# Optimization experiments

Hardware: AMD Instinct MI355X
Metric: run time of the kernel (lower is better)

The kernel has to match this reference:

```python
import jax, jax.numpy as jnp
import numpy as np

H = 16
EPS = 1e-5

def _layernorm(x, gamma, beta):
    mu = jnp.mean(x, axis=-1, keepdims=True)
    var = jnp.var(x, axis=-1, keepdims=True)
    return (x - mu) * jax.lax.rsqrt(var + EPS) * gamma + beta

def setup_inputs() -> dict:
    key = jax.random.key(0)
    ks = jax.random.split(key, 5)
    B, T, E = 4, 2048, 1024
    D = E // H
    return {
        "x": jax.random.normal(ks[0], (B, T, E), dtype=jnp.float32),
        "Wqkv": jax.random.normal(ks[1], (E, 3 * E), dtype=jnp.float32) * (E ** -0.5),
        "bqkv": jax.random.normal(ks[2], (3 * E,), dtype=jnp.float32) * 0.02,
        "q_gamma": jnp.ones((D,), jnp.float32),
        "q_beta": jnp.zeros((D,), jnp.float32),
        "k_gamma": jnp.ones((D,), jnp.float32),
        "k_beta": jnp.zeros((D,), jnp.float32),
        "Wproj": jax.random.normal(ks[3], (E, E), dtype=jnp.float32) * (E ** -0.5),
        "bproj": jnp.zeros((E,), jnp.float32),
    }

def reference(x, Wqkv, bqkv, q_gamma, q_beta, k_gamma, k_beta, Wproj, bproj):
    B, T, E = x.shape
    D = E // H
    qkv = x @ Wqkv + bqkv                      # [B,T,3E]
    q, k, v = jnp.split(qkv, 3, axis=-1)
    # b t (h d) -> b h t d
    to_heads = lambda a: a.reshape(B, T, H, D).transpose(0, 2, 1, 3)
    q, k, v = to_heads(q), to_heads(k), to_heads(v)
    q = _layernorm(q, q_gamma, q_beta)
    k = _layernorm(k, k_gamma, k_beta)
    scale = 1.0 / jnp.sqrt(jnp.float32(D))
    scores = jnp.einsum('bhtd,bhsd->bhts', q, k) * scale   # [B,H,T,T]
    attn = jax.nn.softmax(scores, axis=-1)
    y = jnp.einsum('bhts,bhsd->bhtd', attn, v)             # [B,H,T,D]
    y = y.transpose(0, 2, 1, 3).reshape(B, T, E)           # b h t d -> b t (h d)
    return y @ Wproj + bproj
```

## Files before the change

kernel.cpp:

```cpp
#include <hip/hip_runtime.h>

#define Hn  16
#define Dh  64
#define Bb  4
#define Tn  2048
#define En  1024
#define Mn  8192
#define N1  3072
#define Kn  1024

typedef __attribute__((ext_vector_type(8)))  short  short8;
typedef __attribute__((ext_vector_type(4)))  short  short4v;
typedef __attribute__((ext_vector_type(4)))  float  f32x4;
typedef __attribute__((ext_vector_type(8)))  __bf16 bf16x8;

__device__ __forceinline__ float b2f(short s) {
  unsigned u = ((unsigned)(unsigned short)s) << 16;
  return __builtin_bit_cast(float, u);
}
__device__ __forceinline__ short f2b(float f) {
  unsigned u = __builtin_bit_cast(unsigned, f);
  u += 0x7fffu + ((u >> 16) & 1u);
  return (short)(u >> 16);
}
__device__ __forceinline__ f32x4 mfma16(short8 a, short8 b, f32x4 c) {
  return __builtin_amdgcn_mfma_f32_16x16x32_bf16(
      __builtin_bit_cast(bf16x8, a), __builtin_bit_cast(bf16x8, b), c, 0, 0, 0);
}
__device__ __forceinline__ void gload16(const void* g, void* l) {
  __builtin_amdgcn_global_load_lds(
      (const __attribute__((address_space(1))) unsigned int*)g,
      (__attribute__((address_space(3))) unsigned int*)l, 16, 0, 0);
}

__global__ __launch_bounds__(256) void cvt_x_kernel(const float* __restrict__ x,
                                                    short* __restrict__ xb) {
  const size_t i = ((size_t)blockIdx.x * 256 + threadIdx.x) * 8;
  f32x4 a = *(const f32x4*)&x[i];
  f32x4 b = *(const f32x4*)&x[i + 4];
  short8 o;
  o[0]=f2b(a[0]); o[1]=f2b(a[1]); o[2]=f2b(a[2]); o[3]=f2b(a[3]);
  o[4]=f2b(b[0]); o[5]=f2b(b[1]); o[6]=f2b(b[2]); o[7]=f2b(b[3]);
  *(short8*)&xb[i] = o;
}

__global__ __launch_bounds__(256) void transpose_w_kernel(const float* __restrict__ in,
                                                          short* __restrict__ out,
                                                          int R, int C) {
  __shared__ float tile[32][33];
  const int tid = threadIdx.x;
  const int c0 = blockIdx.x * 32, r0 = blockIdx.y * 32;
  const int lr = tid >> 3, lc = (tid & 7) * 4;
  f32x4 v = *(const f32x4*)&in[(size_t)(r0 + lr) * C + c0 + lc];
  tile[lr][lc] = v[0]; tile[lr][lc+1] = v[1]; tile[lr][lc+2] = v[2]; tile[lr][lc+3] = v[3];
  __syncthreads();
  const int oc = tid >> 3, orr = (tid & 7) * 4;
  short4v ov;
  ov[0] = f2b(tile[orr][oc]);   ov[1] = f2b(tile[orr+1][oc]);
  ov[2] = f2b(tile[orr+2][oc]); ov[3] = f2b(tile[orr+3][oc]);
  *(short4v*)&out[(size_t)(c0 + oc) * R + r0 + orr] = ov;
}

template<int MODE>
__global__ __launch_bounds__(256) void gemm_kernel(
    const short* __restrict__ A, const short* __restrict__ Bt,
    const float* __restrict__ bias, float* __restrict__ Cf,
    short* __restrict__ qo, short* __restrict__ ko2, short* __restrict__ vo,
    const float* __restrict__ qg, const float* __restrict__ qb,
    const float* __restrict__ kg, const float* __restrict__ kb,
    int N, int NBX, int cpx) {
  __shared__ short As[4096];
  __shared__ short Bs[4096];
  const int lin = blockIdx.x;
  const int swz = (lin & 7) * cpx + (lin >> 3);
  const int bx = swz % NBX, by = swz / NBX;
  const int tid = threadIdx.x, lane = tid & 63, w = tid >> 6;
  const int rowBase = by * 128, colBase = bx * 128;
  f32x4 acc[4][4] = {};
  const int srow = tid >> 2, sk = (tid & 3) << 3;
  const short* Ag = A  + (size_t)(rowBase + srow) * Kn + sk;
  const short* Bg = Bt + (size_t)(colBase + srow) * Kn + sk;
  short* AsW = As + w * 512;
  short* BsW = Bs + w * 512;
  const int ar = (w >> 1) * 64, bc = (w & 1) * 64;
  const int lg8 = (lane >> 4) * 8, lr = lane & 15;

  for (int kt = 0; kt < Kn; kt += 32) {
    __syncthreads();
    gload16(Ag + kt,            AsW);
    gload16(Ag + kt + 64 * Kn,  AsW + 2048);
    gload16(Bg + kt,            BsW);
    gload16(Bg + kt + 64 * Kn,  BsW + 2048);
    __syncthreads();
    short8 af[4], bfr[4];
#pragma unroll
    for (int m = 0; m < 4; ++m) af[m]  = *(const short8*)&As[(ar + m*16 + lr)*32 + lg8];
#pragma unroll
    for (int n = 0; n < 4; ++n) bfr[n] = *(const short8*)&Bs[(bc + n*16 + lr)*32 + lg8];
#pragma unroll
    for (int m = 0; m < 4; ++m)
#pragma unroll
      for (int n = 0; n < 4; ++n)
        acc[m][n] = mfma16(af[m], bfr[n], acc[m][n]);
  }

  const int gr0 = rowBase + ar + (lane >> 4) * 4;
  const int gc0 = colBase + bc + lr;

  float bb[4];
#pragma unroll
  for (int n = 0; n < 4; ++n) bb[n] = bias[gc0 + n * 16];
#pragma unroll
  for (int m = 0; m < 4; ++m)
#pragma unroll
    for (int n = 0; n < 4; ++n)
#pragma unroll
      for (int r = 0; r < 4; ++r) acc[m][n][r] += bb[n];

  if (MODE == 1) {
    const int which = colBase >> 10;
    if (which < 2) {
      const float* gp = (which == 0) ? qg : kg;
      const float* bp = (which == 0) ? qb : kb;
      const float sc = (which == 0) ? 0.1803368801111204f : 1.0f;
      float gam[4], bet[4];
#pragma unroll
      for (int n = 0; n < 4; ++n) { gam[n] = gp[n * 16 + lr]; bet[n] = bp[n * 16 + lr]; }
#pragma unroll
      for (int m = 0; m < 4; ++m)
#pragma unroll
        for (int r = 0; r < 4; ++r) {
          float s1 = 0.f, s2 = 0.f;
#pragma unroll
          for (int n = 0; n < 4; ++n) {
            const float v = acc[m][n][r];
            s1 += v; s2 += v * v;
          }
#pragma unroll
          for (int off = 1; off < 16; off <<= 1) {
            s1 += __shfl_xor(s1, off);
            s2 += __shfl_xor(s2, off);
          }
          const float mu = s1 * 0.015625f;
          const float rs = rsqrtf(s2 * 0.015625f - mu * mu + 1e-5f);
#pragma unroll
          for (int n = 0; n < 4; ++n)
            acc[m][n][r] = ((acc[m][n][r] - mu) * rs * gam[n] + bet[n]) * sc;
        }
    }
  }

#pragma unroll
  for (int m = 0; m < 4; ++m) {
#pragma unroll
    for (int n = 0; n < 4; ++n) {
      const int gc = gc0 + n * 16;
#pragma unroll
      for (int r = 0; r < 4; ++r) {
        const int gr = gr0 + m * 16 + r;
        const float v = acc[m][n][r];
        if (MODE == 0) {
          Cf[(size_t)gr * N + gc] = v;
        } else {
          const int which = gc >> 10, e = gc & 1023;
          const int hh = e >> 6, d = e & 63;
          const int bidx = gr >> 11, t = gr & 2047;
          const int bh = bidx * Hn + hh;
          if (which == 0) {
            qo[((size_t)bh * Tn + t) * Dh + d] = f2b(v);
          } else if (which == 1) {
            ko2[((size_t)bh * Tn + t) * Dh + d] = f2b(v);
          } else {
            vo[((size_t)bh * Dh + d) * Tn + t] = f2b(v);
          }
        }
      }
    }
  }
}

__global__ __launch_bounds__(256) void flash_kernel(
    const short* __restrict__ qp, const short* __restrict__ kp,
    const short* __restrict__ vt, short* __restrict__ y) {
  __shared__ short Ks[2][4096];
  __shared__ short Vs[2][4096];
  __shared__ short Ps[4096];
  const int tid = threadIdx.x, lane = tid & 63, w = tid >> 6;
  const int lr = lane & 15, lg = lane >> 4;

  const int j0 = blockIdx.x;
  const int xcd = j0 & 7, kk0 = j0 >> 3;
  const int bh = 8 * xcd + (kk0 & 7), qt = kk0 >> 3;

  const int qrow0 = qt * 128 + w * 32;
  const short* qbase = qp + ((size_t)bh * Tn + qrow0) * Dh;

  short8 aq[2][2];
#pragma unroll
  for (int m = 0; m < 2; ++m)
#pragma unroll
    for (int kk = 0; kk < 2; ++kk)
      aq[m][kk] = *(const short8*)&qbase[(m*16 + lr)*64 + kk*32 + lg*8];

  short8 ones;
#pragma unroll
  for (int i = 0; i < 8; ++i) ones[i] = (short)0x3F80;

  f32x4 o[2][4] = {};
  f32x4 lacc[2] = {};
  float mrow[2][4];
#pragma unroll
  for (int m = 0; m < 2; ++m)
#pragma unroll
    for (int r = 0; r < 4; ++r) mrow[m][r] = -3e38f;

  const int srow = tid >> 3;
  const int sc = (tid & 7) * 8;
  short* Pw = Ps + w * 1024;
  const short* kb = kp + (size_t)bh * Tn * Dh;
  const short* vb = vt + (size_t)bh * Dh * Tn;

#define STAGE(jt, bsel)                                                   \
  {                                                                       \
    _Pragma("unroll")                                                     \
    for (int i = 0; i < 2; ++i) {                                         \
      const int row = i * 32 + srow;                                      \
      const int scs = sc ^ ((row & 7) << 3);                              \
      gload16(kb + (size_t)((jt) * 64 + row) * Dh + scs,                  \
              &Ks[bsel][w * 512 + i * 2048]);                             \
      gload16(vb + (size_t)row * Tn + (jt) * 64 + scs,                    \
              &Vs[bsel][w * 512 + i * 2048]);                             \
    }                                                                     \
  }

#define PSW(q) ((((q) & 3) << 3) ^ (((q) & 4) << 2))

  STAGE(0, 0);
  __syncthreads();

  for (int j = 0; j < Tn / 64; ++j) {
    const int cur = j & 1;
    if (j + 1 < Tn / 64) STAGE(j + 1, cur ^ 1);

    short8 bk[4][2];
#pragma unroll
    for (int n = 0; n < 4; ++n)
#pragma unroll
      for (int kk = 0; kk < 2; ++kk) {
        const int row = n * 16 + lr;
        bk[n][kk] = *(const short8*)&Ks[cur][row*64 + ((kk*32 + lg*8) ^ ((row & 7) << 3))];
      }
    f32x4 s[2][4] = {};
    __builtin_amdgcn_s_setprio(1);
#pragma unroll
    for (int m = 0; m < 2; ++m)
#pragma unroll
      for (int n = 0; n < 4; ++n) {
        s[m][n] = mfma16(aq[m][0], bk[n][0], s[m][n]);
        s[m][n] = mfma16(aq[m][1], bk[n][1], s[m][n]);
      }
    __builtin_amdgcn_s_setprio(0);

    float pm[2][4];
#pragma unroll
    for (int m = 0; m < 2; ++m)
#pragma unroll
      for (int r = 0; r < 4; ++r)
        pm[m][r] = fmaxf(fmaxf(s[m][0][r], s[m][1][r]), fmaxf(s[m][2][r], s[m][3][r]));
    int ok = 1;
#pragma unroll
    for (int m = 0; m < 2; ++m)
#pragma unroll
      for (int r = 0; r < 4; ++r)
        ok &= (pm[m][r] <= mrow[m][r] + 11.0f) ? 1 : 0;
    if (!__all(ok)) {
      float tm[2][4];
#pragma unroll
      for (int m = 0; m < 2; ++m)
#pragma unroll
        for (int r = 0; r < 4; ++r) tm[m][r] = pm[m][r];
#pragma unroll
      for (int off = 1; off < 16; off <<= 1)
#pragma unroll
        for (int m = 0; m < 2; ++m)
#pragma unroll
          for (int r = 0; r < 4; ++r)
            tm[m][r] = fmaxf(tm[m][r], __shfl_xor(tm[m][r], off));
#pragma unroll
      for (int m = 0; m < 2; ++m)
#pragma unroll
        for (int r = 0; r < 4; ++r) {
          const float mn = fmaxf(mrow[m][r], tm[m][r]);
          const float corr = __builtin_amdgcn_exp2f(mrow[m][r] - mn);
          lacc[m][r] *= corr;
#pragma unroll
          for (int dn = 0; dn < 4; ++dn) o[m][dn][r] *= corr;
          mrow[m][r] = mn;
        }
    }

    short8 bv[4][2];
#pragma unroll
    for (int dn = 0; dn < 4; ++dn)
#pragma unroll
      for (int kk = 0; kk < 2; ++kk) {
        const int row = dn * 16 + lr;
        bv[dn][kk] = *(const short8*)&Vs[cur][row*64 + ((kk*32 + lg*8) ^ ((row & 7) << 3))];
      }

    __syncthreads();

#pragma unroll
    for (int m = 0; m < 2; ++m)
#pragma unroll
      for (int n = 0; n < 2; ++n)
#pragma unroll
        for (int r = 0; r < 4; ++r) {
          const float p = __builtin_amdgcn_exp2f(s[m][n][r] - mrow[m][r]);
          const unsigned u = __builtin_bit_cast(unsigned, p);
          const int q = m*16 + lg*4 + r;
          Pw[q*32 + ((n*16 + lr) ^ PSW(q))] = (short)(u >> 16);
        }
    short8 pa0[2];
#pragma unroll
    for (int m = 0; m < 2; ++m) {
      const int q = m*16 + lr;
      pa0[m] = *(const short8*)&Pw[q*32 + ((lg*8) ^ PSW(q))];
    }
    __builtin_amdgcn_s_setprio(1);
#pragma unroll
    for (int m = 0; m < 2; ++m) {
      lacc[m] = mfma16(pa0[m], ones, lacc[m]);
#pragma unroll
      for (int dn = 0; dn < 4; ++dn)
        o[m][dn] = mfma16(pa0[m], bv[dn][0], o[m][dn]);
    }
    __builtin_amdgcn_s_setprio(0);

#pragma unroll
    for (int m = 0; m < 2; ++m)
#pragma unroll
      for (int n = 0; n < 2; ++n)
#pragma unroll
        for (int r = 0; r < 4; ++r) {
          const float p = __builtin_amdgcn_exp2f(s[m][2 + n][r] - mrow[m][r]);
          const unsigned u = __builtin_bit_cast(unsigned, p);
          const int q = m*16 + lg*4 + r;
          Pw[q*32 + ((n*16 + lr) ^ PSW(q))] = (short)(u >> 16);
        }
    short8 pa1[2];
#pragma unroll
    for (int m = 0; m < 2; ++m) {
      const int q = m*16 + lr;
      pa1[m] = *(const short8*)&Pw[q*32 + ((lg*8) ^ PSW(q))];
    }
    __builtin_amdgcn_s_setprio(1);
#pragma unroll
    for (int m = 0; m < 2; ++m) {
      lacc[m] = mfma16(pa1[m], ones, lacc[m]);
#pragma unroll
      for (int dn = 0; dn < 4; ++dn)
        o[m][dn] = mfma16(pa1[m], bv[dn][1], o[m][dn]);
    }
    __builtin_amdgcn_s_setprio(0);
  }
#undef STAGE
#undef PSW

  const int b = bh >> 4, hh = bh & 15;
  short* yb = y + (size_t)b * Tn * En + hh * 64;
#pragma unroll
  for (int m = 0; m < 2; ++m)
#pragma unroll
    for (int r = 0; r < 4; ++r) {
      const float rl = 1.0f / lacc[m][r];
      const int t = qrow0 + m*16 + lg*4 + r;
#pragma unroll
      for (int dn = 0; dn < 4; ++dn) {
        const int d = dn*16 + lr;
        yb[(size_t)t * En + d] = f2b(o[m][dn][r] * rl);
      }
    }
}

extern "C" void kernel_launch(void* const* d_in, const int* in_sizes, int n_in,
                              void* d_out, int out_size, void* d_ws, size_t ws_size,
                              hipStream_t stream) {
  const float* x     = (const float*)d_in[0];
  const float* Wqkv  = (const float*)d_in[1];
  const float* bqkv  = (const float*)d_in[2];
  const float* qg    = (const float*)d_in[3];
  const float* qb    = (const float*)d_in[4];
  const float* kg    = (const float*)d_in[5];
  const float* kb    = (const float*)d_in[6];
  const float* Wproj = (const float*)d_in[7];
  const float* bproj = (const float*)d_in[8];
  float* out = (float*)d_out;

  char* p = (char*)d_ws;
  short* xb     = (short*)p; p += (size_t)Mn * Kn * 2;
  short* wqkvT  = (short*)p; p += (size_t)N1 * Kn * 2;
  short* wprojT = (short*)p; p += (size_t)En * Kn * 2;
  short* qp     = (short*)p; p += (size_t)Mn * Kn * 2;
  short* kp     = (short*)p; p += (size_t)Mn * Kn * 2;
  short* vtb    = (short*)p; p += (size_t)Mn * Kn * 2;
  short* yb     = (short*)p; p += (size_t)Mn * Kn * 2;

  cvt_x_kernel<<<Mn * Kn / (256 * 8), 256, 0, stream>>>(x, xb);
  transpose_w_kernel<<<dim3(N1 / 32, Kn / 32), 256, 0, stream>>>(Wqkv, wqkvT, Kn, N1);
  transpose_w_kernel<<<dim3(En / 32, Kn / 32), 256, 0, stream>>>(Wproj, wprojT, Kn, En);
  gemm_kernel<1><<<(N1 / 128) * (Mn / 128), 256, 0, stream>>>(
      xb, wqkvT, bqkv, nullptr, qp, kp, vtb, qg, qb, kg, kb,
      N1, N1 / 128, (N1 / 128) * (Mn / 128) / 8);
  flash_kernel<<<1024, 256, 0, stream>>>(qp, kp, vtb, yb);
  gemm_kernel<0><<<(En / 128) * (Mn / 128), 256, 0, stream>>>(
      yb, wprojT, bproj, out, nullptr, nullptr, nullptr, nullptr, nullptr, nullptr, nullptr,
      En, En / 128, (En / 128) * (Mn / 128) / 8);
}
```

Baseline: 264.5 us.

## Stage QKV epilogue through swizzled LDS for vectorized stores; merge prep kernels

The QKV GEMM epilogue now converts each wave's accumulators to bf16 into a swizzled LDS tile, then writes Q, K and transposed V with 16-byte vector stores. Before, it issued scattered 2-byte stores, and the V-transpose stores were strided. The three preprocessing kernels (x conversion and the two weight transposes) are merged into one launch. The change adds an extra barrier and LDS round trip in the epilogue, and reuses the GEMM's shared buffer for staging.

```diff
diff --git a/kernel.cpp b/kernel.cpp
--- a/kernel.cpp
+++ b/kernel.cpp
@@ -33,23 +33,31 @@
       (__attribute__((address_space(3))) unsigned int*)l, 16, 0, 0);
 }
 
-__global__ __launch_bounds__(256) void cvt_x_kernel(const float* __restrict__ x,
-                                                    short* __restrict__ xb) {
-  const size_t i = ((size_t)blockIdx.x * 256 + threadIdx.x) * 8;
-  f32x4 a = *(const f32x4*)&x[i];
-  f32x4 b = *(const f32x4*)&x[i + 4];
-  short8 o;
-  o[0]=f2b(a[0]); o[1]=f2b(a[1]); o[2]=f2b(a[2]); o[3]=f2b(a[3]);
-  o[4]=f2b(b[0]); o[5]=f2b(b[1]); o[6]=f2b(b[2]); o[7]=f2b(b[3]);
-  *(short8*)&xb[i] = o;
-}
-
-__global__ __launch_bounds__(256) void transpose_w_kernel(const float* __restrict__ in,
-                                                          short* __restrict__ out,
-                                                          int R, int C) {
+__global__ __launch_bounds__(256) void prep_kernel(
+    const float* __restrict__ x, short* __restrict__ xb,
+    const float* __restrict__ Wqkv, short* __restrict__ wqkvT,
+    const float* __restrict__ Wproj, short* __restrict__ wprojT) {
   __shared__ float tile[32][33];
-  const int tid = threadIdx.x;
-  const int c0 = blockIdx.x * 32, r0 = blockIdx.y * 32;
+  const int bid = blockIdx.x, tid = threadIdx.x;
+  if (bid < 4096) {
+    const size_t i = ((size_t)bid * 256 + tid) * 8;
+    f32x4 a = *(const f32x4*)&x[i];
+    f32x4 b = *(const f32x4*)&x[i + 4];
+    short8 o;
+    o[0]=f2b(a[0]); o[1]=f2b(a[1]); o[2]=f2b(a[2]); o[3]=f2b(a[3]);
+    o[4]=f2b(b[0]); o[5]=f2b(b[1]); o[6]=f2b(b[2]); o[7]=f2b(b[3]);
+    *(short8*)&xb[i] = o;
+    return;
+  }
+  const float* in; short* out; int R, C, bx, by;
+  if (bid < 4096 + 3072) {
+    const int b2 = bid - 4096;
+    in = Wqkv; out = wqkvT; R = Kn; C = N1; bx = b2 % 96; by = b2 / 96;
+  } else {
+    const int b3 = bid - 7168;
+    in = Wproj; out = wprojT; R = Kn; C = En; bx = b3 % 32; by = b3 / 32;
+  }
+  const int c0 = bx * 32, r0 = by * 32;
   const int lr = tid >> 3, lc = (tid & 7) * 4;
   f32x4 v = *(const f32x4*)&in[(size_t)(r0 + lr) * C + c0 + lc];
   tile[lr][lc] = v[0]; tile[lr][lc+1] = v[1]; tile[lr][lc+2] = v[2]; tile[lr][lc+3] = v[3];
@@ -69,8 +77,7 @@
     const float* __restrict__ qg, const float* __restrict__ qb,
     const float* __restrict__ kg, const float* __restrict__ kb,
     int N, int NBX, int cpx) {
-  __shared__ short As[4096];
-  __shared__ short Bs[4096];
+  __shared__ short S[8192];
   const int lin = blockIdx.x;
   const int swz = (lin & 7) * cpx + (lin >> 3);
   const int bx = swz % NBX, by = swz / NBX;
@@ -80,10 +87,10 @@
   const int srow = tid >> 2, sk = (tid & 3) << 3;
   const short* Ag = A  + (size_t)(rowBase + srow) * Kn + sk;
   const short* Bg = Bt + (size_t)(colBase + srow) * Kn + sk;
-  short* AsW = As + w * 512;
-  short* BsW = Bs + w * 512;
+  short* AsW = S + w * 512;
+  short* BsW = S + 4096 + w * 512;
   const int ar = (w >> 1) * 64, bc = (w & 1) * 64;
-  const int lg8 = (lane >> 4) * 8, lr = lane & 15;
+  const int lg = lane >> 4, lg8 = lg * 8, lr = lane & 15;
 
   for (int kt = 0; kt < Kn; kt += 32) {
     __syncthreads();
@@ -94,9 +101,9 @@
     __syncthreads();
     short8 af[4], bfr[4];
 #pragma unroll
-    for (int m = 0; m < 4; ++m) af[m]  = *(const short8*)&As[(ar + m*16 + lr)*32 + lg8];
-#pragma unroll
-    for (int n = 0; n < 4; ++n) bfr[n] = *(const short8*)&Bs[(bc + n*16 + lr)*32 + lg8];
+    for (int m = 0; m < 4; ++m) af[m]  = *(const short8*)&S[(ar + m*16 + lr)*32 + lg8];
+#pragma unroll
+    for (int n = 0; n < 4; ++n) bfr[n] = *(const short8*)&S[4096 + (bc + n*16 + lr)*32 + lg8];
 #pragma unroll
     for (int m = 0; m < 4; ++m)
 #pragma unroll
@@ -104,7 +111,7 @@
         acc[m][n] = mfma16(af[m], bfr[n], acc[m][n]);
   }
 
-  const int gr0 = rowBase + ar + (lane >> 4) * 4;
+  const int gr0 = rowBase + ar + lg * 4;
   const int gc0 = colBase + bc + lr;
 
   float bb[4];
@@ -117,63 +124,103 @@
 #pragma unroll
       for (int r = 0; r < 4; ++r) acc[m][n][r] += bb[n];
 
-  if (MODE == 1) {
-    const int which = colBase >> 10;
-    if (which < 2) {
-      const float* gp = (which == 0) ? qg : kg;
-      const float* bp = (which == 0) ? qb : kb;
-      const float sc = (which == 0) ? 0.1803368801111204f : 1.0f;
-      float gam[4], bet[4];
-#pragma unroll
-      for (int n = 0; n < 4; ++n) { gam[n] = gp[n * 16 + lr]; bet[n] = bp[n * 16 + lr]; }
-#pragma unroll
-      for (int m = 0; m < 4; ++m)
-#pragma unroll
-        for (int r = 0; r < 4; ++r) {
-          float s1 = 0.f, s2 = 0.f;
-#pragma unroll
-          for (int n = 0; n < 4; ++n) {
-            const float v = acc[m][n][r];
-            s1 += v; s2 += v * v;
+  if (MODE == 0) {
+#pragma unroll
+    for (int m = 0; m < 4; ++m)
+#pragma unroll
+      for (int n = 0; n < 4; ++n) {
+        const int gc = gc0 + n * 16;
+#pragma unroll
+        for (int r = 0; r < 4; ++r)
+          Cf[(size_t)(gr0 + m*16 + r) * N + gc] = acc[m][n][r];
+      }
+    return;
+  }
+
+  const int which = colBase >> 10;
+  if (which < 2) {
+    const float* gp = (which == 0) ? qg : kg;
+    const float* bp = (which == 0) ? qb : kb;
+    const float sc = (which == 0) ? 0.1803368801111204f : 1.0f;
+    float gam[4], bet[4];
+#pragma unroll
+    for (int n = 0; n < 4; ++n) { gam[n] = gp[n * 16 + lr]; bet[n] = bp[n * 16 + lr]; }
+#pragma unroll
+    for (int m = 0; m < 4; ++m)
+#pragma unroll
+      for (int r = 0; r < 4; ++r) {
+        float s1 = 0.f, s2 = 0.f;
+#pragma unroll
+        for (int n = 0; n < 4; ++n) {
+          const float v = acc[m][n][r];
+          s1 += v; s2 += v * v;
+        }
+#pragma unroll
+        for (int off = 1; off < 16; off <<= 1) {
+          s1 += __shfl_xor(s1, off);
+          s2 += __shfl_xor(s2, off);
+        }
+        const float mu = s1 * 0.015625f;
+        const float rs = rsqrtf(s2 * 0.015625f - mu * mu + 1e-5f);
+#pragma unroll
+        for (int n = 0; n < 4; ++n)
+          acc[m][n][r] = ((acc[m][n][r] - mu) * rs * gam[n] + bet[n]) * sc;
+      }
+  }
+
+  __syncthreads();
+  short* Sw = S + w * 2048;
+  const int t0 = (rowBase & 2047) + ar;
+  const int bidx = (rowBase + ar) >> 11;
+  const int hh = ((colBase + bc) & 1023) >> 6;
+  const int bh = bidx * Hn + hh;
+  const int l8 = lane & 7, ld8 = lane >> 3;
+
+  if (which < 2) {
+    short* dst0 = (which == 0) ? qo : ko2;
+#pragma unroll
+    for (int p = 0; p < 2; ++p) {
+#pragma unroll
+      for (int mm = 0; mm < 2; ++mm) {
+        const int m = p * 2 + mm;
+#pragma unroll
+        for (int n = 0; n < 4; ++n)
+#pragma unroll
+          for (int r = 0; r < 4; ++r) {
+            const int tl = mm*16 + lg*4 + r;
+            const int dl = n*16 + lr;
+            Sw[tl*64 + (dl ^ ((tl & 7) << 3))] = f2b(acc[m][n][r]);
           }
-#pragma unroll
-          for (int off = 1; off < 16; off <<= 1) {
-            s1 += __shfl_xor(s1, off);
-            s2 += __shfl_xor(s2, off);
+      }
+#pragma unroll
+      for (int i = 0; i < 4; ++i) {
+        const int tl = i*8 + ld8;
+        short8 v = *(const short8*)&Sw[tl*64 + ((l8*8) ^ ((tl & 7) << 3))];
+        const int t = t0 + p*32 + tl;
+        *(short8*)&dst0[((size_t)bh * Tn + t) * Dh + l8*8] = v;
+      }
+    }
+  } else {
+#pragma unroll
+    for (int p = 0; p < 2; ++p) {
+#pragma unroll
+      for (int nn = 0; nn < 2; ++nn) {
+        const int n = p * 2 + nn;
+#pragma unroll
+        for (int m = 0; m < 4; ++m)
+#pragma unroll
+          for (int r = 0; r < 4; ++r) {
+            const int dl = nn*16 + lr;
+            const int tc = m*16 + lg*4 + r;
+            Sw[dl*64 + (tc ^ ((dl & 7) << 3))] = f2b(acc[m][n][r]);
           }
-          const float mu = s1 * 0.015625f;
-          const float rs = rsqrtf(s2 * 0.015625f - mu * mu + 1e-5f);
-#pragma unroll
-          for (int n = 0; n < 4; ++n)
-            acc[m][n][r] = ((acc[m][n][r] - mu) * rs * gam[n] + bet[n]) * sc;
-        }
-    }
-  }
-
-#pragma unroll
-  for (int m = 0; m < 4; ++m) {
-#pragma unroll
-    for (int n = 0; n < 4; ++n) {
-      const int gc = gc0 + n * 16;
-#pragma unroll
-      for (int r = 0; r < 4; ++r) {
-        const int gr = gr0 + m * 16 + r;
-        const float v = acc[m][n][r];
-        if (MODE == 0) {
-          Cf[(size_t)gr * N + gc] = v;
-        } else {
-          const int which = gc >> 10, e = gc & 1023;
-          const int hh = e >> 6, d = e & 63;
-          const int bidx = gr >> 11, t = gr & 2047;
-          const int bh = bidx * Hn + hh;
-          if (which == 0) {
-            qo[((size_t)bh * Tn + t) * Dh + d] = f2b(v);
-          } else if (which == 1) {
-            ko2[((size_t)bh * Tn + t) * Dh + d] = f2b(v);
-          } else {
-            vo[((size_t)bh * Dh + d) * Tn + t] = f2b(v);
-          }
-        }
+      }
+#pragma unroll
+      for (int i = 0; i < 4; ++i) {
+        const int dl = i*8 + ld8;
+        short8 v = *(const short8*)&Sw[dl*64 + ((l8*8) ^ ((dl & 7) << 3))];
+        const int d = p*32 + dl;
+        *(short8*)&vo[((size_t)bh * Dh + d) * Tn + t0 + l8*8] = v;
       }
     }
   }
@@ -406,9 +453,7 @@
   short* vtb    = (short*)p; p += (size_t)Mn * Kn * 2;
   short* yb     = (short*)p; p += (size_t)Mn * Kn * 2;
 
-  cvt_x_kernel<<<Mn * Kn / (256 * 8), 256, 0, stream>>>(x, xb);
-  transpose_w_kernel<<<dim3(N1 / 32, Kn / 32), 256, 0, stream>>>(Wqkv, wqkvT, Kn, N1);
-  transpose_w_kernel<<<dim3(En / 32, Kn / 32), 256, 0, stream>>>(Wproj, wprojT, Kn, En);
+  prep_kernel<<<8192, 256, 0, stream>>>(x, xb, Wqkv, wqkvT, Wproj, wprojT);
   gemm_kernel<1><<<(N1 / 128) * (Mn / 128), 256, 0, stream>>>(
       xb, wqkvT, bqkv, nullptr, qp, kp, vtb, qg, qb, kg, kb,
       N1, N1 / 128, (N1 / 128) * (Mn / 128) / 8);
```

Result: faster. 245.6 us (-7.2%).
